# Kernel optimization log

Hardware: AMD Instinct MI355X
Metric: run time of the kernel (lower is better)

## Reference

```python
import jax, jax.numpy as jnp
import numpy as np

B, S, E, H = 4, 1024, 1024, 16
DK = E // H
NEG = -10000.0


def setup_inputs() -> dict:
    key = jax.random.key(0)
    ks = jax.random.split(key, 8)
    x = jax.random.normal(ks[0], (B, S, E), dtype=jnp.float32)
    # causal additive mask [S, S]: 0 on/below diagonal, -10000 above
    causal = jnp.where(jnp.triu(jnp.ones((S, S), dtype=bool), k=1), NEG, 0.0).astype(jnp.float32)
    # key padding mask [B, S]: True = PAD. Random valid lengths per batch row.
    lengths = jax.random.randint(ks[1], (B,), S // 2, S + 1)
    key_padding_mask = jnp.arange(S)[None, :] >= lengths[:, None]
    # Linear params (torch Linear: y = x @ W.T + b)
    sc = 1.0 / np.sqrt(E)
    qkv_w = jax.random.uniform(ks[2], (3 * E, E), minval=-sc, maxval=sc, dtype=jnp.float32)
    qkv_b = jax.random.uniform(ks[3], (3 * E,), minval=-sc, maxval=sc, dtype=jnp.float32)
    out_w = jax.random.uniform(ks[4], (E, E), minval=-sc, maxval=sc, dtype=jnp.float32)
    out_b = jax.random.uniform(ks[5], (E,), minval=-sc, maxval=sc, dtype=jnp.float32)
    return {"x": x, "attn_mask": causal, "key_padding_mask": key_padding_mask,
            "qkv_w": qkv_w, "qkv_b": qkv_b, "out_w": out_w, "out_b": out_b}


def reference(x, attn_mask, key_padding_mask, qkv_w, qkv_b, out_w, out_b):
    b, s, _ = x.shape
    qkv = x @ qkv_w.T + qkv_b                     # [b, s, 3E]
    q, k, v = jnp.split(qkv, 3, axis=-1)
    # [b, H, s, d_k]
    q = q.reshape(b, s, H, DK).transpose(0, 2, 1, 3)
    k = k.reshape(b, s, H, DK).transpose(0, 2, 1, 3)
    v = v.reshape(b, s, H, DK).transpose(0, 2, 1, 3)
    pad = key_padding_mask[:, None, :, None]       # [b, 1, s, 1]
    q = jnp.where(pad, 0.0, q)
    k = jnp.where(pad, 0.0, k)
    v = jnp.where(pad, 0.0, v)
    scores = jnp.einsum('bhqd,bhkd->bhqk', q, k) / jnp.sqrt(jnp.float32(DK))
    scores = scores + attn_mask[None, None, :, :]  # additive causal mask
    scores = jnp.where(key_padding_mask[:, None, None, :], NEG, scores)
    attn_weights = jax.nn.softmax(scores, axis=-1)  # [b, H, s, s]
    attn_output = jnp.einsum('bhqk,bhkd->bhqd', attn_weights, v)
    attn_output = attn_output.transpose(0, 2, 1, 3).reshape(b, s, E)
    attn_output = attn_output @ out_w.T + out_b
    return attn_output, attn_weights
```

## Files before the change

kernel.cpp:

```cpp
#include <hip/hip_runtime.h>
#include <math.h>

namespace {
constexpr int Bn = 4, Sn = 1024, En = 1024, Hn = 16, DKn = 64;
constexpr float NEGV = -10000.0f;
constexpr float SCALE = 0.125f;
constexpr int LDR = 40;
constexpr int LDK = 72;
constexpr int LDP = 136;
}

typedef __attribute__((ext_vector_type(8))) short bf16x8;
typedef __attribute__((ext_vector_type(4))) float f32x4;

__device__ inline short f2b(float f) {
  unsigned u = __builtin_bit_cast(unsigned, f);
  u += 0x7fffu + ((u >> 16) & 1u);
  return (short)(u >> 16);
}
__device__ inline float b2f(short s) {
  return __builtin_bit_cast(float, ((unsigned)(unsigned short)s) << 16);
}

__global__ __launch_bounds__(256) void cast_kernel(const float* __restrict__ in,
                                                   short* __restrict__ out, int n4) {
  int i = blockIdx.x * 256 + threadIdx.x;
  if (i < n4) {
    float4 v = ((const float4*)in)[i];
    short4 o = {f2b(v.x), f2b(v.y), f2b(v.z), f2b(v.w)};
    ((short4*)out)[i] = o;
  }
}

__global__ __launch_bounds__(256) void qkv_mfma_kernel(
    const short* __restrict__ xb, const short* __restrict__ wb,
    const float* __restrict__ bias, const int* __restrict__ kpm,
    short* __restrict__ qb, short* __restrict__ kb, short* __restrict__ vtb) {
  __shared__ short As[128 * LDR];
  __shared__ short Bs[128 * LDR];
  const int tid = threadIdx.x;
  const int wave = tid >> 6, lane = tid & 63;
  const int quad = lane >> 4, l16 = lane & 15;
  const int wm = (wave >> 1) * 64, wn = (wave & 1) * 64;
  const int m0 = blockIdx.y * 128, n0 = blockIdx.x * 128;
  const int srow = tid >> 2, scol = (tid & 3) * 8;
  f32x4 acc[4][4];
#pragma unroll
  for (int i = 0; i < 4; ++i)
#pragma unroll
    for (int j = 0; j < 4; ++j) acc[i][j] = (f32x4){0.f, 0.f, 0.f, 0.f};
  for (int k0 = 0; k0 < 1024; k0 += 32) {
    bf16x8 a0 = *(const bf16x8*)(xb + (size_t)(m0 + srow) * 1024 + k0 + scol);
    bf16x8 a1 = *(const bf16x8*)(xb + (size_t)(m0 + srow + 64) * 1024 + k0 + scol);
    bf16x8 b0 = *(const bf16x8*)(wb + (size_t)(n0 + srow) * 1024 + k0 + scol);
    bf16x8 b1 = *(const bf16x8*)(wb + (size_t)(n0 + srow + 64) * 1024 + k0 + scol);
    __syncthreads();
    *(bf16x8*)(As + srow * LDR + scol) = a0;
    *(bf16x8*)(As + (srow + 64) * LDR + scol) = a1;
    *(bf16x8*)(Bs + srow * LDR + scol) = b0;
    *(bf16x8*)(Bs + (srow + 64) * LDR + scol) = b1;
    __syncthreads();
    bf16x8 af[4], bfv[4];
#pragma unroll
    for (int i = 0; i < 4; ++i)
      af[i] = *(const bf16x8*)(As + (wm + i * 16 + l16) * LDR + quad * 8);
#pragma unroll
    for (int j = 0; j < 4; ++j)
      bfv[j] = *(const bf16x8*)(Bs + (wn + j * 16 + l16) * LDR + quad * 8);
#pragma unroll
    for (int i = 0; i < 4; ++i)
#pragma unroll
      for (int j = 0; j < 4; ++j)
        acc[i][j] = __builtin_amdgcn_mfma_f32_16x16x32_bf16(af[i], bfv[j], acc[i][j], 0, 0, 0);
  }
  const int bidx = m0 >> 10;
  const int which = n0 >> 10;
  if (which == 2) {
#pragma unroll
    for (int j = 0; j < 4; ++j) {
      const int gn = n0 + wn + j * 16 + l16;
      const int e = gn & 1023, h = e >> 6, d = e & 63;
      const float bb = bias[gn];
      const size_t bh = (size_t)(bidx * Hn + h);
#pragma unroll
      for (int i = 0; i < 4; ++i) {
        const int gm0 = m0 + wm + i * 16 + quad * 4;
        const int s0 = gm0 & 1023;
        short4 o;
        {
          const bool k0m = kpm[gm0 + 0] != 0;
          const bool k1m = kpm[gm0 + 1] != 0;
          const bool k2m = kpm[gm0 + 2] != 0;
          const bool k3m = kpm[gm0 + 3] != 0;
          o.x = f2b(k0m ? 0.f : acc[i][j][0] + bb);
          o.y = f2b(k1m ? 0.f : acc[i][j][1] + bb);
          o.z = f2b(k2m ? 0.f : acc[i][j][2] + bb);
          o.w = f2b(k3m ? 0.f : acc[i][j][3] + bb);
        }
        *(short4*)(vtb + (bh * 64 + d) * 1024 + s0) = o;
      }
    }
  } else {
    short* dst = (which == 0) ? qb : kb;
#pragma unroll
    for (int j = 0; j < 4; ++j) {
      const int gn = n0 + wn + j * 16 + l16;
      const int e = gn & 1023, h = e >> 6, d = e & 63;
      const float bb = bias[gn];
      const size_t bh = (size_t)(bidx * Hn + h);
#pragma unroll
      for (int i = 0; i < 4; ++i) {
#pragma unroll
        for (int r = 0; r < 4; ++r) {
          const int gm = m0 + wm + i * 16 + quad * 4 + r;
          const int s = gm & 1023;
          const bool msk = kpm[gm] != 0;
          dst[(bh * 1024 + s) * 64 + d] = f2b(msk ? 0.f : acc[i][j][r] + bb);
        }
      }
    }
  }
}

__global__ __launch_bounds__(256, 2) void attn_fused_kernel(
    const short* __restrict__ qb, const short* __restrict__ kb,
    const short* __restrict__ vtb, const int* __restrict__ kpm,
    float* __restrict__ wout, short* __restrict__ apb) {
  __shared__ short Ks[128 * LDK];
  __shared__ short Vs[64 * LDP];
  __shared__ short Ps[128 * LDP];
  __shared__ int kpms[1024];
  const int bh = blockIdx.y, bidx = bh >> 4, h = bh & 15;
  const int qt = (blockIdx.y >= 32) ? (7 - (int)blockIdx.x) : (int)blockIdx.x;
  const int q0 = qt * 128;
  const int ntiles = qt + 1;
  const short* Q = qb + (size_t)bh * Sn * DKn;
  const short* K = kb + (size_t)bh * Sn * DKn;
  const short* V = vtb + (size_t)bh * DKn * Sn;
  const int tid = threadIdx.x;
  const int wave = tid >> 6, lane = tid & 63, quad = lane >> 4, l16 = lane & 15;
  const int wrow = wave * 32;
  for (int i = tid; i < 1024; i += 256) kpms[i] = kpm[bidx * Sn + i];
  bf16x8 qf[2][2];
#pragma unroll
  for (int i = 0; i < 2; ++i) {
    const int row = q0 + wrow + i * 16 + l16;
#pragma unroll
    for (int s = 0; s < 2; ++s)
      qf[i][s] = *(const bf16x8*)(Q + (size_t)row * 64 + s * 32 + quad * 8);
  }
  float l8[8];
#pragma unroll
  for (int i = 0; i < 8; ++i) l8[i] = 0.f;

  for (int t = 0; t < ntiles; ++t) {
    const int k0 = t * 128;
    __syncthreads();
    {
      const int r = tid >> 1, c0 = (tid & 1) * 32;
      const short* src = K + (size_t)(k0 + r) * 64 + c0;
      short* dst = Ks + r * LDK + c0;
#pragma unroll
      for (int u = 0; u < 4; ++u)
        *(bf16x8*)(dst + u * 8) = *(const bf16x8*)(src + u * 8);
    }
    __syncthreads();
    f32x4 sc[2][8];
#pragma unroll
    for (int i = 0; i < 2; ++i)
#pragma unroll
      for (int j = 0; j < 8; ++j) sc[i][j] = (f32x4){0.f, 0.f, 0.f, 0.f};
#pragma unroll
    for (int s = 0; s < 2; ++s) {
      bf16x8 bk[8];
#pragma unroll
      for (int j = 0; j < 8; ++j)
        bk[j] = *(const bf16x8*)(Ks + (j * 16 + l16) * LDK + s * 32 + quad * 8);
#pragma unroll
      for (int i = 0; i < 2; ++i)
#pragma unroll
        for (int j = 0; j < 8; ++j)
          sc[i][j] = __builtin_amdgcn_mfma_f32_16x16x32_bf16(qf[i][s], bk[j], sc[i][j], 0, 0, 0);
    }
    int cm[8];
#pragma unroll
    for (int j = 0; j < 8; ++j) cm[j] = kpms[k0 + j * 16 + l16];
    const bool diag = (t == qt);
#pragma unroll
    for (int i = 0; i < 2; ++i)
#pragma unroll
      for (int r = 0; r < 4; ++r) {
        const int idx = i * 4 + r;
        const int row = q0 + wrow + i * 16 + quad * 4 + r;
        float sum = 0.f;
#pragma unroll
        for (int j = 0; j < 8; ++j) {
          const int col = k0 + j * 16 + l16;
          float s = sc[i][j][r] * SCALE;
          if (cm[j]) s = NEGV;
          if (diag && col > row) s = NEGV;
          sum += __expf(s);
        }
#pragma unroll
        for (int d = 1; d < 16; d <<= 1) sum += __shfl_xor(sum, d);
        l8[idx] += sum;
      }
  }
  float linv[8];
#pragma unroll
  for (int i = 0; i < 8; ++i) linv[i] = 1.0f / l8[i];

  f32x4 oacc[2][4];
#pragma unroll
  for (int i = 0; i < 2; ++i)
#pragma unroll
    for (int j = 0; j < 4; ++j) oacc[i][j] = (f32x4){0.f, 0.f, 0.f, 0.f};
  for (int t = 0; t < ntiles; ++t) {
    const int k0 = t * 128;
    __syncthreads();
    {
      const int r = tid >> 1, c0 = (tid & 1) * 32;
      const short* src = K + (size_t)(k0 + r) * 64 + c0;
      short* dst = Ks + r * LDK + c0;
#pragma unroll
      for (int u = 0; u < 4; ++u)
        *(bf16x8*)(dst + u * 8) = *(const bf16x8*)(src + u * 8);
    }
    {
      const int vr = tid >> 2, c0 = (tid & 3) * 32;
      const short* src = V + (size_t)vr * Sn + k0 + c0;
      short* dst = Vs + vr * LDP + c0;
#pragma unroll
      for (int u = 0; u < 4; ++u)
        *(bf16x8*)(dst + u * 8) = *(const bf16x8*)(src + u * 8);
    }
    __syncthreads();
    f32x4 sc[2][8];
#pragma unroll
    for (int i = 0; i < 2; ++i)
#pragma unroll
      for (int j = 0; j < 8; ++j) sc[i][j] = (f32x4){0.f, 0.f, 0.f, 0.f};
#pragma unroll
    for (int s = 0; s < 2; ++s) {
      bf16x8 bk[8];
#pragma unroll
      for (int j = 0; j < 8; ++j)
        bk[j] = *(const bf16x8*)(Ks + (j * 16 + l16) * LDK + s * 32 + quad * 8);
#pragma unroll
      for (int i = 0; i < 2; ++i)
#pragma unroll
        for (int j = 0; j < 8; ++j)
          sc[i][j] = __builtin_amdgcn_mfma_f32_16x16x32_bf16(qf[i][s], bk[j], sc[i][j], 0, 0, 0);
    }
    int cm[8];
#pragma unroll
    for (int j = 0; j < 8; ++j) cm[j] = kpms[k0 + j * 16 + l16];
    const bool diag = (t == qt);
#pragma unroll
    for (int i = 0; i < 2; ++i)
#pragma unroll
      for (int r = 0; r < 4; ++r) {
        const int idx = i * 4 + r;
        const int row = q0 + wrow + i * 16 + quad * 4 + r;
        const int rloc = wrow + i * 16 + quad * 4 + r;
#pragma unroll
        for (int j = 0; j < 8; ++j) {
          const int col = k0 + j * 16 + l16;
          float s = sc[i][j][r] * SCALE;
          if (cm[j]) s = NEGV;
          if (diag && col > row) s = NEGV;
          Ps[rloc * LDP + j * 16 + l16] = f2b(__expf(s) * linv[idx]);
        }
      }
    __syncthreads();
#pragma unroll
    for (int s4 = 0; s4 < 4; ++s4) {
      bf16x8 pa[2], vb[4];
#pragma unroll
      for (int i = 0; i < 2; ++i)
        pa[i] = *(const bf16x8*)(Ps + (wrow + i * 16 + l16) * LDP + s4 * 32 + quad * 8);
#pragma unroll
      for (int j = 0; j < 4; ++j)
        vb[j] = *(const bf16x8*)(Vs + (j * 16 + l16) * LDP + s4 * 32 + quad * 8);
#pragma unroll
      for (int i = 0; i < 2; ++i)
#pragma unroll
        for (int j = 0; j < 4; ++j)
          oacc[i][j] = __builtin_amdgcn_mfma_f32_16x16x32_bf16(pa[i], vb[j], oacc[i][j], 0, 0, 0);
    }
#pragma unroll 4
    for (int g = 0; g < 16; ++g) {
      const int unit = g * 256 + tid;
      const int row = unit >> 5, c4 = unit & 31;
      short4 s4v = *(const short4*)(Ps + row * LDP + c4 * 4);
      float4 o = {b2f(s4v.x), b2f(s4v.y), b2f(s4v.z), b2f(s4v.w)};
      *(float4*)(wout + ((size_t)bh * Sn + q0 + row) * Sn + k0 + c4 * 4) = o;
    }
  }
  const int zc0 = ntiles * 128;
  const int span4 = (Sn - zc0) >> 2;
  const float4 z4 = {0.f, 0.f, 0.f, 0.f};
  for (int r = 0; r < 128; ++r)
    for (int c = tid; c < span4; c += 256)
      ((float4*)(wout + ((size_t)bh * Sn + q0 + r) * Sn + zc0))[c] = z4;
#pragma unroll
  for (int i = 0; i < 2; ++i)
#pragma unroll
    for (int j = 0; j < 4; ++j)
#pragma unroll
      for (int r = 0; r < 4; ++r) {
        const int s = q0 + wrow + i * 16 + quad * 4 + r;
        apb[((size_t)(bidx * Sn + s)) * En + h * 64 + j * 16 + l16] = f2b(oacc[i][j][r]);
      }
}

__global__ __launch_bounds__(256) void out_mfma_kernel(
    const short* __restrict__ ab, const short* __restrict__ wb,
    const float* __restrict__ bias, float* __restrict__ out) {
  __shared__ short As[128 * LDR];
  __shared__ short Bs[128 * LDR];
  const int tid = threadIdx.x;
  const int wave = tid >> 6, lane = tid & 63;
  const int quad = lane >> 4, l16 = lane & 15;
  const int wm = (wave >> 1) * 64, wn = (wave & 1) * 64;
  const int m0 = blockIdx.y * 128, n0 = blockIdx.x * 128;
  const int srow = tid >> 2, scol = (tid & 3) * 8;
  f32x4 acc[4][4];
#pragma unroll
  for (int i = 0; i < 4; ++i)
#pragma unroll
    for (int j = 0; j < 4; ++j) acc[i][j] = (f32x4){0.f, 0.f, 0.f, 0.f};
  for (int k0 = 0; k0 < 1024; k0 += 32) {
    bf16x8 a0 = *(const bf16x8*)(ab + (size_t)(m0 + srow) * 1024 + k0 + scol);
    bf16x8 a1 = *(const bf16x8*)(ab + (size_t)(m0 + srow + 64) * 1024 + k0 + scol);
    bf16x8 b0 = *(const bf16x8*)(wb + (size_t)(n0 + srow) * 1024 + k0 + scol);
    bf16x8 b1 = *(const bf16x8*)(wb + (size_t)(n0 + srow + 64) * 1024 + k0 + scol);
    __syncthreads();
    *(bf16x8*)(As + srow * LDR + scol) = a0;
    *(bf16x8*)(As + (srow + 64) * LDR + scol) = a1;
    *(bf16x8*)(Bs + srow * LDR + scol) = b0;
    *(bf16x8*)(Bs + (srow + 64) * LDR + scol) = b1;
    __syncthreads();
    bf16x8 af[4], bfv[4];
#pragma unroll
    for (int i = 0; i < 4; ++i)
      af[i] = *(const bf16x8*)(As + (wm + i * 16 + l16) * LDR + quad * 8);
#pragma unroll
    for (int j = 0; j < 4; ++j)
      bfv[j] = *(const bf16x8*)(Bs + (wn + j * 16 + l16) * LDR + quad * 8);
#pragma unroll
    for (int i = 0; i < 4; ++i)
#pragma unroll
      for (int j = 0; j < 4; ++j)
        acc[i][j] = __builtin_amdgcn_mfma_f32_16x16x32_bf16(af[i], bfv[j], acc[i][j], 0, 0, 0);
  }
#pragma unroll
  for (int j = 0; j < 4; ++j) {
    const int gn = n0 + wn + j * 16 + l16;
    const float bb = bias[gn];
#pragma unroll
    for (int i = 0; i < 4; ++i) {
#pragma unroll
      for (int r = 0; r < 4; ++r) {
        const int gm = m0 + wm + i * 16 + quad * 4 + r;
        out[(size_t)gm * 1024 + gn] = acc[i][j][r] + bb;
      }
    }
  }
}

extern "C" void kernel_launch(void* const* d_in, const int* in_sizes, int n_in,
                              void* d_out, int out_size, void* d_ws, size_t ws_size,
                              hipStream_t stream) {
  const float* x        = (const float*)d_in[0];
  const int*   kpm      = (const int*)d_in[2];
  const float* qkv_w    = (const float*)d_in[3];
  const float* qkv_b    = (const float*)d_in[4];
  const float* out_w    = (const float*)d_in[5];
  const float* out_b    = (const float*)d_in[6];

  float* out     = (float*)d_out;
  float* weights = out + (size_t)Bn * Sn * En;

  short* ws  = (short*)d_ws;
  short* xb  = ws;
  short* wqb = xb  + ((size_t)4 << 20);
  short* owb = wqb + ((size_t)3 << 20);
  short* qb  = owb + ((size_t)1 << 20);
  short* kb  = qb  + ((size_t)4 << 20);
  short* vtb = kb  + ((size_t)4 << 20);
  short* apb = vtb + ((size_t)4 << 20);

  cast_kernel<<<4096, 256, 0, stream>>>(x, xb, 1 << 20);
  cast_kernel<<<3072, 256, 0, stream>>>(qkv_w, wqb, 3 << 18);
  cast_kernel<<<1024, 256, 0, stream>>>(out_w, owb, 1 << 18);
  qkv_mfma_kernel<<<dim3(24, 32), 256, 0, stream>>>(xb, wqb, qkv_b, kpm, qb, kb, vtb);
  attn_fused_kernel<<<dim3(8, 64), 256, 0, stream>>>(qb, kb, vtb, kpm, weights, apb);
  out_mfma_kernel<<<dim3(8, 32), 256, 0, stream>>>(apb, owb, out_b, out);
}
```

Before: 461.6 us.

## Merge cast kernels, widen attention to 512 threads with transposed MFMA

Folds the three fp32-to-bf16 casts into one launch. The attention kernel now runs 512 threads, each wave owning 16 query rows. It swaps the MFMA operands so every lane holds one query row, which makes row sums need only two shuffles and lets P and the output be stored as short4 vectors. The output projection also swaps its MFMA operands so results go out as float4 stores. The trade-off is more threads per block and a different register and LDS access pattern, including possible bank conflicts on the per-lane Ps writes.

Measured after the change: 422.5 us. 8.5% less time.

```diff
diff --git a/kernel.cpp b/kernel.cpp
--- a/kernel.cpp
+++ b/kernel.cpp
@@ -22,14 +22,20 @@
   return __builtin_bit_cast(float, ((unsigned)(unsigned short)s) << 16);
 }
 
-__global__ __launch_bounds__(256) void cast_kernel(const float* __restrict__ in,
-                                                   short* __restrict__ out, int n4) {
-  int i = blockIdx.x * 256 + threadIdx.x;
-  if (i < n4) {
-    float4 v = ((const float4*)in)[i];
-    short4 o = {f2b(v.x), f2b(v.y), f2b(v.z), f2b(v.w)};
-    ((short4*)out)[i] = o;
-  }
+__global__ __launch_bounds__(256) void cast3_kernel(
+    const float* __restrict__ x, const float* __restrict__ w1,
+    const float* __restrict__ w2, short* __restrict__ xb,
+    short* __restrict__ wb1, short* __restrict__ wb2) {
+  const int b = blockIdx.x, tid = threadIdx.x;
+  const float* src;
+  short* dst;
+  int i;
+  if (b < 4096) { src = x;  dst = xb;  i = b * 256 + tid; }
+  else if (b < 7168) { src = w1; dst = wb1; i = (b - 4096) * 256 + tid; }
+  else { src = w2; dst = wb2; i = (b - 7168) * 256 + tid; }
+  float4 v = ((const float4*)src)[i];
+  short4 o = {f2b(v.x), f2b(v.y), f2b(v.z), f2b(v.w)};
+  ((short4*)dst)[i] = o;
 }
 
 __global__ __launch_bounds__(256) void qkv_mfma_kernel(
@@ -87,16 +93,10 @@
         const int gm0 = m0 + wm + i * 16 + quad * 4;
         const int s0 = gm0 & 1023;
         short4 o;
-        {
-          const bool k0m = kpm[gm0 + 0] != 0;
-          const bool k1m = kpm[gm0 + 1] != 0;
-          const bool k2m = kpm[gm0 + 2] != 0;
-          const bool k3m = kpm[gm0 + 3] != 0;
-          o.x = f2b(k0m ? 0.f : acc[i][j][0] + bb);
-          o.y = f2b(k1m ? 0.f : acc[i][j][1] + bb);
-          o.z = f2b(k2m ? 0.f : acc[i][j][2] + bb);
-          o.w = f2b(k3m ? 0.f : acc[i][j][3] + bb);
-        }
+        o.x = f2b(kpm[gm0 + 0] ? 0.f : acc[i][j][0] + bb);
+        o.y = f2b(kpm[gm0 + 1] ? 0.f : acc[i][j][1] + bb);
+        o.z = f2b(kpm[gm0 + 2] ? 0.f : acc[i][j][2] + bb);
+        o.w = f2b(kpm[gm0 + 3] ? 0.f : acc[i][j][3] + bb);
         *(short4*)(vtb + (bh * 64 + d) * 1024 + s0) = o;
       }
     }
@@ -114,15 +114,14 @@
         for (int r = 0; r < 4; ++r) {
           const int gm = m0 + wm + i * 16 + quad * 4 + r;
           const int s = gm & 1023;
-          const bool msk = kpm[gm] != 0;
-          dst[(bh * 1024 + s) * 64 + d] = f2b(msk ? 0.f : acc[i][j][r] + bb);
+          dst[(bh * 1024 + s) * 64 + d] = f2b(kpm[gm] ? 0.f : acc[i][j][r] + bb);
         }
       }
     }
   }
 }
 
-__global__ __launch_bounds__(256, 2) void attn_fused_kernel(
+__global__ __launch_bounds__(512, 4) void attn_fused_kernel(
     const short* __restrict__ qb, const short* __restrict__ kb,
     const short* __restrict__ vtb, const int* __restrict__ kpm,
     float* __restrict__ wout, short* __restrict__ apb) {
@@ -139,37 +138,29 @@
   const short* V = vtb + (size_t)bh * DKn * Sn;
   const int tid = threadIdx.x;
   const int wave = tid >> 6, lane = tid & 63, quad = lane >> 4, l16 = lane & 15;
-  const int wrow = wave * 32;
-  for (int i = tid; i < 1024; i += 256) kpms[i] = kpm[bidx * Sn + i];
-  bf16x8 qf[2][2];
-#pragma unroll
-  for (int i = 0; i < 2; ++i) {
-    const int row = q0 + wrow + i * 16 + l16;
-#pragma unroll
-    for (int s = 0; s < 2; ++s)
-      qf[i][s] = *(const bf16x8*)(Q + (size_t)row * 64 + s * 32 + quad * 8);
-  }
-  float l8[8];
-#pragma unroll
-  for (int i = 0; i < 8; ++i) l8[i] = 0.f;
+  const int qloc = wave * 16 + l16;
+  const int qe = q0 + qloc;
+  for (int i = tid; i < 1024; i += 512) kpms[i] = kpm[bidx * Sn + i];
+  bf16x8 qf[2];
+#pragma unroll
+  for (int s = 0; s < 2; ++s)
+    qf[s] = *(const bf16x8*)(Q + (size_t)qe * 64 + s * 32 + quad * 8);
+  float l = 0.f;
 
   for (int t = 0; t < ntiles; ++t) {
     const int k0 = t * 128;
     __syncthreads();
     {
-      const int r = tid >> 1, c0 = (tid & 1) * 32;
+      const int r = tid >> 2, c0 = (tid & 3) * 16;
       const short* src = K + (size_t)(k0 + r) * 64 + c0;
       short* dst = Ks + r * LDK + c0;
-#pragma unroll
-      for (int u = 0; u < 4; ++u)
-        *(bf16x8*)(dst + u * 8) = *(const bf16x8*)(src + u * 8);
-    }
-    __syncthreads();
-    f32x4 sc[2][8];
-#pragma unroll
-    for (int i = 0; i < 2; ++i)
-#pragma unroll
-      for (int j = 0; j < 8; ++j) sc[i][j] = (f32x4){0.f, 0.f, 0.f, 0.f};
+      *(bf16x8*)(dst) = *(const bf16x8*)(src);
+      *(bf16x8*)(dst + 8) = *(const bf16x8*)(src + 8);
+    }
+    __syncthreads();
+    f32x4 sc[8];
+#pragma unroll
+    for (int j = 0; j < 8; ++j) sc[j] = (f32x4){0.f, 0.f, 0.f, 0.f};
 #pragma unroll
     for (int s = 0; s < 2; ++s) {
       bf16x8 bk[8];
@@ -177,69 +168,54 @@
       for (int j = 0; j < 8; ++j)
         bk[j] = *(const bf16x8*)(Ks + (j * 16 + l16) * LDK + s * 32 + quad * 8);
 #pragma unroll
-      for (int i = 0; i < 2; ++i)
-#pragma unroll
-        for (int j = 0; j < 8; ++j)
-          sc[i][j] = __builtin_amdgcn_mfma_f32_16x16x32_bf16(qf[i][s], bk[j], sc[i][j], 0, 0, 0);
-    }
-    int cm[8];
-#pragma unroll
-    for (int j = 0; j < 8; ++j) cm[j] = kpms[k0 + j * 16 + l16];
+      for (int j = 0; j < 8; ++j)
+        sc[j] = __builtin_amdgcn_mfma_f32_16x16x32_bf16(bk[j], qf[s], sc[j], 0, 0, 0);
+    }
     const bool diag = (t == qt);
-#pragma unroll
-    for (int i = 0; i < 2; ++i)
+    float sum = 0.f;
+#pragma unroll
+    for (int j = 0; j < 8; ++j) {
+      const int kbase = k0 + j * 16 + quad * 4;
+      const int4 cmv = *(const int4*)&kpms[kbase];
+      const int cmr[4] = {cmv.x, cmv.y, cmv.z, cmv.w};
 #pragma unroll
       for (int r = 0; r < 4; ++r) {
-        const int idx = i * 4 + r;
-        const int row = q0 + wrow + i * 16 + quad * 4 + r;
-        float sum = 0.f;
-#pragma unroll
-        for (int j = 0; j < 8; ++j) {
-          const int col = k0 + j * 16 + l16;
-          float s = sc[i][j][r] * SCALE;
-          if (cm[j]) s = NEGV;
-          if (diag && col > row) s = NEGV;
-          sum += __expf(s);
-        }
-#pragma unroll
-        for (int d = 1; d < 16; d <<= 1) sum += __shfl_xor(sum, d);
-        l8[idx] += sum;
+        float s = sc[j][r] * SCALE;
+        if (cmr[r]) s = NEGV;
+        if (diag && (kbase + r) > qe) s = NEGV;
+        sum += __expf(s);
       }
-  }
-  float linv[8];
-#pragma unroll
-  for (int i = 0; i < 8; ++i) linv[i] = 1.0f / l8[i];
-
-  f32x4 oacc[2][4];
-#pragma unroll
-  for (int i = 0; i < 2; ++i)
-#pragma unroll
-    for (int j = 0; j < 4; ++j) oacc[i][j] = (f32x4){0.f, 0.f, 0.f, 0.f};
+    }
+    sum += __shfl_xor(sum, 16);
+    sum += __shfl_xor(sum, 32);
+    l += sum;
+  }
+  const float linv = 1.0f / l;
+
+  f32x4 oacc[4];
+#pragma unroll
+  for (int j = 0; j < 4; ++j) oacc[j] = (f32x4){0.f, 0.f, 0.f, 0.f};
   for (int t = 0; t < ntiles; ++t) {
     const int k0 = t * 128;
     __syncthreads();
     {
-      const int r = tid >> 1, c0 = (tid & 1) * 32;
+      const int r = tid >> 2, c0 = (tid & 3) * 16;
       const short* src = K + (size_t)(k0 + r) * 64 + c0;
       short* dst = Ks + r * LDK + c0;
-#pragma unroll
-      for (int u = 0; u < 4; ++u)
-        *(bf16x8*)(dst + u * 8) = *(const bf16x8*)(src + u * 8);
+      *(bf16x8*)(dst) = *(const bf16x8*)(src);
+      *(bf16x8*)(dst + 8) = *(const bf16x8*)(src + 8);
     }
     {
-      const int vr = tid >> 2, c0 = (tid & 3) * 32;
+      const int vr = tid >> 3, c0 = (tid & 7) * 16;
       const short* src = V + (size_t)vr * Sn + k0 + c0;
       short* dst = Vs + vr * LDP + c0;
-#pragma unroll
-      for (int u = 0; u < 4; ++u)
-        *(bf16x8*)(dst + u * 8) = *(const bf16x8*)(src + u * 8);
-    }
-    __syncthreads();
-    f32x4 sc[2][8];
-#pragma unroll
-    for (int i = 0; i < 2; ++i)
-#pragma unroll
-      for (int j = 0; j < 8; ++j) sc[i][j] = (f32x4){0.f, 0.f, 0.f, 0.f};
+      *(bf16x8*)(dst) = *(const bf16x8*)(src);
+      *(bf16x8*)(dst + 8) = *(const bf16x8*)(src + 8);
+    }
+    __syncthreads();
+    f32x4 sc[8];
+#pragma unroll
+    for (int j = 0; j < 8; ++j) sc[j] = (f32x4){0.f, 0.f, 0.f, 0.f};
 #pragma unroll
     for (int s = 0; s < 2; ++s) {
       bf16x8 bk[8];
@@ -247,50 +223,42 @@
       for (int j = 0; j < 8; ++j)
         bk[j] = *(const bf16x8*)(Ks + (j * 16 + l16) * LDK + s * 32 + quad * 8);
 #pragma unroll
-      for (int i = 0; i < 2; ++i)
-#pragma unroll
-        for (int j = 0; j < 8; ++j)
-          sc[i][j] = __builtin_amdgcn_mfma_f32_16x16x32_bf16(qf[i][s], bk[j], sc[i][j], 0, 0, 0);
-    }
-    int cm[8];
-#pragma unroll
-    for (int j = 0; j < 8; ++j) cm[j] = kpms[k0 + j * 16 + l16];
+      for (int j = 0; j < 8; ++j)
+        sc[j] = __builtin_amdgcn_mfma_f32_16x16x32_bf16(bk[j], qf[s], sc[j], 0, 0, 0);
+    }
     const bool diag = (t == qt);
 #pragma unroll
-    for (int i = 0; i < 2; ++i)
+    for (int j = 0; j < 8; ++j) {
+      const int kbase = k0 + j * 16 + quad * 4;
+      const int4 cmv = *(const int4*)&kpms[kbase];
+      const int cmr[4] = {cmv.x, cmv.y, cmv.z, cmv.w};
+      short4 o;
+      float p[4];
 #pragma unroll
       for (int r = 0; r < 4; ++r) {
-        const int idx = i * 4 + r;
-        const int row = q0 + wrow + i * 16 + quad * 4 + r;
-        const int rloc = wrow + i * 16 + quad * 4 + r;
-#pragma unroll
-        for (int j = 0; j < 8; ++j) {
-          const int col = k0 + j * 16 + l16;
-          float s = sc[i][j][r] * SCALE;
-          if (cm[j]) s = NEGV;
-          if (diag && col > row) s = NEGV;
-          Ps[rloc * LDP + j * 16 + l16] = f2b(__expf(s) * linv[idx]);
-        }
+        float s = sc[j][r] * SCALE;
+        if (cmr[r]) s = NEGV;
+        if (diag && (kbase + r) > qe) s = NEGV;
+        p[r] = __expf(s) * linv;
       }
+      o.x = f2b(p[0]); o.y = f2b(p[1]); o.z = f2b(p[2]); o.w = f2b(p[3]);
+      *(short4*)(Ps + qloc * LDP + j * 16 + quad * 4) = o;
+    }
     __syncthreads();
 #pragma unroll
     for (int s4 = 0; s4 < 4; ++s4) {
-      bf16x8 pa[2], vb[4];
-#pragma unroll
-      for (int i = 0; i < 2; ++i)
-        pa[i] = *(const bf16x8*)(Ps + (wrow + i * 16 + l16) * LDP + s4 * 32 + quad * 8);
+      bf16x8 pa = *(const bf16x8*)(Ps + qloc * LDP + s4 * 32 + quad * 8);
+      bf16x8 vb[4];
 #pragma unroll
       for (int j = 0; j < 4; ++j)
         vb[j] = *(const bf16x8*)(Vs + (j * 16 + l16) * LDP + s4 * 32 + quad * 8);
 #pragma unroll
-      for (int i = 0; i < 2; ++i)
-#pragma unroll
-        for (int j = 0; j < 4; ++j)
-          oacc[i][j] = __builtin_amdgcn_mfma_f32_16x16x32_bf16(pa[i], vb[j], oacc[i][j], 0, 0, 0);
-    }
-#pragma unroll 4
-    for (int g = 0; g < 16; ++g) {
-      const int unit = g * 256 + tid;
+      for (int j = 0; j < 4; ++j)
+        oacc[j] = __builtin_amdgcn_mfma_f32_16x16x32_bf16(vb[j], pa, oacc[j], 0, 0, 0);
+    }
+#pragma unroll
+    for (int g = 0; g < 8; ++g) {
+      const int unit = g * 512 + tid;
       const int row = unit >> 5, c4 = unit & 31;
       short4 s4v = *(const short4*)(Ps + row * LDP + c4 * 4);
       float4 o = {b2f(s4v.x), b2f(s4v.y), b2f(s4v.z), b2f(s4v.w)};
@@ -301,17 +269,15 @@
   const int span4 = (Sn - zc0) >> 2;
   const float4 z4 = {0.f, 0.f, 0.f, 0.f};
   for (int r = 0; r < 128; ++r)
-    for (int c = tid; c < span4; c += 256)
+    for (int c = tid; c < span4; c += 512)
       ((float4*)(wout + ((size_t)bh * Sn + q0 + r) * Sn + zc0))[c] = z4;
 #pragma unroll
-  for (int i = 0; i < 2; ++i)
-#pragma unroll
-    for (int j = 0; j < 4; ++j)
-#pragma unroll
-      for (int r = 0; r < 4; ++r) {
-        const int s = q0 + wrow + i * 16 + quad * 4 + r;
-        apb[((size_t)(bidx * Sn + s)) * En + h * 64 + j * 16 + l16] = f2b(oacc[i][j][r]);
-      }
+  for (int j = 0; j < 4; ++j) {
+    short4 o;
+    o.x = f2b(oacc[j][0]); o.y = f2b(oacc[j][1]);
+    o.z = f2b(oacc[j][2]); o.w = f2b(oacc[j][3]);
+    *(short4*)(apb + ((size_t)(bidx * Sn + qe)) * En + h * 64 + j * 16 + quad * 4) = o;
+  }
 }
 
 __global__ __launch_bounds__(256) void out_mfma_kernel(
@@ -352,19 +318,21 @@
     for (int i = 0; i < 4; ++i)
 #pragma unroll
       for (int j = 0; j < 4; ++j)
-        acc[i][j] = __builtin_amdgcn_mfma_f32_16x16x32_bf16(af[i], bfv[j], acc[i][j], 0, 0, 0);
-  }
-#pragma unroll
-  for (int j = 0; j < 4; ++j) {
-    const int gn = n0 + wn + j * 16 + l16;
-    const float bb = bias[gn];
-#pragma unroll
-    for (int i = 0; i < 4; ++i) {
-#pragma unroll
-      for (int r = 0; r < 4; ++r) {
-        const int gm = m0 + wm + i * 16 + quad * 4 + r;
-        out[(size_t)gm * 1024 + gn] = acc[i][j][r] + bb;
-      }
+        acc[i][j] = __builtin_amdgcn_mfma_f32_16x16x32_bf16(bfv[j], af[i], acc[i][j], 0, 0, 0);
+  }
+  float4 bb4[4];
+#pragma unroll
+  for (int j = 0; j < 4; ++j)
+    bb4[j] = *(const float4*)&bias[n0 + wn + j * 16 + quad * 4];
+#pragma unroll
+  for (int i = 0; i < 4; ++i) {
+    const int gm = m0 + wm + i * 16 + l16;
+#pragma unroll
+    for (int j = 0; j < 4; ++j) {
+      const int gn0 = n0 + wn + j * 16 + quad * 4;
+      float4 o = {acc[i][j][0] + bb4[j].x, acc[i][j][1] + bb4[j].y,
+                  acc[i][j][2] + bb4[j].z, acc[i][j][3] + bb4[j].w};
+      *(float4*)(out + (size_t)gm * 1024 + gn0) = o;
     }
   }
 }
@@ -391,10 +359,8 @@
   short* vtb = kb  + ((size_t)4 << 20);
   short* apb = vtb + ((size_t)4 << 20);
 
-  cast_kernel<<<4096, 256, 0, stream>>>(x, xb, 1 << 20);
-  cast_kernel<<<3072, 256, 0, stream>>>(qkv_w, wqb, 3 << 18);
-  cast_kernel<<<1024, 256, 0, stream>>>(out_w, owb, 1 << 18);
+  cast3_kernel<<<8192, 256, 0, stream>>>(x, qkv_w, out_w, xb, wqb, owb);
   qkv_mfma_kernel<<<dim3(24, 32), 256, 0, stream>>>(xb, wqb, qkv_b, kpm, qb, kb, vtb);
-  attn_fused_kernel<<<dim3(8, 64), 256, 0, stream>>>(qb, kb, vtb, kpm, weights, apb);
+  attn_fused_kernel<<<dim3(8, 64), 512, 0, stream>>>(qb, kb, vtb, kpm, weights, apb);
   out_mfma_kernel<<<dim3(8, 32), 256, 0, stream>>>(apb, owb, out_b, out);
 }
```
